# Kernel tuning notes

Hardware: AMD Instinct MI355X
Metric: run time of the kernel (lower is better)

The kernel has to match this reference:

```python
import jax, jax.numpy as jnp
import numpy as np

N_NODES = 100000

def _gcn_conv(x, W, b, src, dst, ew, num_nodes):
    # x: [N, Fin], W: [Fin, Fout], src/dst: [Etot], ew: [Etot]
    xw = x @ W                                   # [N, Fout]
    deg = jax.ops.segment_sum(ew, dst, num_segments=num_nodes)   # [N]
    dinv = jnp.where(deg > 0, jax.lax.rsqrt(jnp.where(deg > 0, deg, 1.0)), 0.0)
    norm = dinv[src] * ew * dinv[dst]            # [Etot]
    msg = xw[src] * norm[:, None]                # [Etot, Fout] gather-transform
    out = jax.ops.segment_sum(msg, dst, num_segments=num_nodes)  # scatter-add
    return out + b

def setup_inputs() -> dict:
    key = jax.random.key(0)
    k1, k2, k3, k4, k5, k6, k7 = jax.random.split(key, 7)
    N, E, F_IN, HID, CLS = N_NODES, 1600000, 128, 64, 32
    x = jax.random.normal(k1, (N, F_IN), dtype=jnp.float32)
    edge_index = jax.random.randint(k2, (2, E), 0, N, dtype=jnp.int64)
    edge_weight = jax.random.uniform(k3, (E,), dtype=jnp.float32)
    s1 = 1.0 / np.sqrt(F_IN)
    s2 = 1.0 / np.sqrt(HID)
    W1 = jax.random.uniform(k4, (F_IN, HID), dtype=jnp.float32, minval=-s1, maxval=s1)
    b1 = jnp.zeros((HID,), dtype=jnp.float32)
    W2 = jax.random.uniform(k5, (HID, CLS), dtype=jnp.float32, minval=-s2, maxval=s2)
    b2 = jnp.zeros((CLS,), dtype=jnp.float32)
    return {"x": x, "edge_index": edge_index, "edge_weight": edge_weight,
            "W1": W1, "b1": b1, "W2": W2, "b2": b2}

def reference(x, edge_index, edge_weight, W1, b1, W2, b2):
    N = x.shape[0]
    # add self-loops with weight 1 (PyG GCNConv default)
    loop = jnp.arange(N, dtype=edge_index.dtype)
    src = jnp.concatenate([edge_index[0], loop])
    dst = jnp.concatenate([edge_index[1], loop])
    ew = jnp.concatenate([edge_weight, jnp.ones((N,), dtype=edge_weight.dtype)])
    h = _gcn_conv(x, W1, b1, src, dst, ew, N)
    h = jax.nn.relu(h)
    # dropout is identity in eval mode
    out = _gcn_conv(h, W2, b2, src, dst, ew, N)
    return out
```

## Files before the change

### kernel.cpp

```cpp
#include <hip/hip_runtime.h>

#define FIN 128
#define HID 64
#define CLS 32

#define BSH 7
#define BNODES 128
#define GB 256
#define BCAP 4096
#define SCAP 6272
#define NBUKP 800

using bfrag = __attribute__((ext_vector_type(8))) short;
using cfrag = __attribute__((ext_vector_type(4))) float;

__device__ inline unsigned short f2bf(float x) {
  unsigned u = __float_as_uint(x);
  return (unsigned short)((u + 0x7FFFu + ((u >> 16) & 1u)) >> 16);
}
__device__ inline void bf8_to_f32(int4 v, float* f) {
  f[0] = __uint_as_float((unsigned)v.x << 16);
  f[1] = __uint_as_float((unsigned)v.x & 0xFFFF0000u);
  f[2] = __uint_as_float((unsigned)v.y << 16);
  f[3] = __uint_as_float((unsigned)v.y & 0xFFFF0000u);
  f[4] = __uint_as_float((unsigned)v.z << 16);
  f[5] = __uint_as_float((unsigned)v.z & 0xFFFF0000u);
  f[6] = __uint_as_float((unsigned)v.w << 16);
  f[7] = __uint_as_float((unsigned)v.w & 0xFFFF0000u);
}

__global__ __launch_bounds__(256) void k_wpack(const float* __restrict__ W1,
                                               const float* __restrict__ W2,
                                               unsigned short* __restrict__ wp1,
                                               unsigned short* __restrict__ wp2) {
  int t = blockIdx.x * 256 + threadIdx.x;
  int total = gridDim.x * 256;
  for (int i = t; i < 16 * 512; i += total) {
    int f = i >> 9, l = (i >> 3) & 63, j = i & 7;
    int ks = f >> 2, nt = f & 3;
    int k = ks * 32 + (l >> 4) * 8 + j;
    int n = nt * 16 + (l & 15);
    wp1[i] = f2bf(W1[k * 64 + n]);
  }
  for (int i = t; i < 4 * 512; i += total) {
    int f = i >> 9, l = (i >> 3) & 63, j = i & 7;
    int ks = f >> 1, nt = f & 1;
    int k = ks * 32 + (l >> 4) * 8 + j;
    int n = nt * 16 + (l & 15);
    wp2[i] = f2bf(W2[k * 32 + n]);
  }
}

__global__ __launch_bounds__(1024) void k_sortchunk(const int* __restrict__ src,
                                                    const int* __restrict__ dst,
                                                    const float* __restrict__ ew,
                                                    int2* __restrict__ recsA,
                                                    int* __restrict__ gcntT,
                                                    int* __restrict__ loffB,
                                                    int E, int CHUNK, int NBUK) {
  __shared__ int2 stage[SCAP];
  __shared__ int lcnt[NBUKP];
  __shared__ int loff[NBUKP];
  __shared__ int lcur[NBUKP];
  __shared__ int ssum[1024];
  const int b = blockIdx.x, t = threadIdx.x;
  const int s = b * CHUNK, e = min(E, s + CHUNK);
  const int m = e - s;

  for (int i = t; i < NBUK; i += 1024) lcnt[i] = 0;
  __syncthreads();
  for (int p = s + t; p < e; p += 1024)
    atomicAdd(&lcnt[dst[p] >> BSH], 1);
  __syncthreads();

  int c = (t < NBUK) ? lcnt[t] : 0;
  ssum[t] = c;
  __syncthreads();
  for (int off = 1; off < 1024; off <<= 1) {
    int v = (t >= off) ? ssum[t - off] : 0;
    __syncthreads();
    ssum[t] += v;
    __syncthreads();
  }
  if (t < NBUK) { loff[t] = ssum[t] - c; lcur[t] = ssum[t] - c; }
  if (t == 0) loff[NBUK] = m;
  __syncthreads();

  for (int p = s + t; p < e; p += 1024) {
    int d = dst[p];
    int bk = d >> BSH;
    int pos = atomicAdd(&lcur[bk], 1);
    stage[pos] = make_int2(src[p] | ((d & (BNODES - 1)) << 17), __float_as_int(ew[p]));
  }
  __syncthreads();

  for (int p = t; p < m; p += 1024) recsA[s + p] = stage[p];
  for (int i = t; i < NBUK; i += 1024) gcntT[i * GB + b] = lcnt[i];
  for (int i = t; i <= NBUK; i += 1024) loffB[b * NBUKP + i] = loff[i];
}

__global__ __launch_bounds__(256) void k_scan_sums(const int* __restrict__ counts,
                                                   int* __restrict__ bsum, int N) {
  __shared__ int s[256];
  int base = blockIdx.x * 4096 + threadIdx.x * 16;
  int t = 0;
#pragma unroll
  for (int j = 0; j < 16; ++j)
    if (base + j < N) t += counts[base + j];
  s[threadIdx.x] = t;
  __syncthreads();
  for (int off = 128; off > 0; off >>= 1) {
    if (threadIdx.x < off) s[threadIdx.x] += s[threadIdx.x + off];
    __syncthreads();
  }
  if (threadIdx.x == 0) bsum[blockIdx.x] = s[0];
}

__global__ __launch_bounds__(256) void k_scan_bsums(int* __restrict__ bsum, int nb) {
  __shared__ int s[256];
  int t = threadIdx.x;
  int v = (t < nb) ? bsum[t] : 0;
  s[t] = v;
  __syncthreads();
  for (int off = 1; off < 256; off <<= 1) {
    int u = (t >= off) ? s[t - off] : 0;
    __syncthreads();
    s[t] += u;
    __syncthreads();
  }
  if (t < nb) bsum[t] = s[t] - v;
}

__global__ __launch_bounds__(256) void k_scan_emit(const int* __restrict__ counts,
                                                   const int* __restrict__ bsum,
                                                   int* __restrict__ rowstart, int N) {
  __shared__ int s[256];
  int base = blockIdx.x * 4096 + threadIdx.x * 16;
  int c[16];
  int tsum = 0;
#pragma unroll
  for (int j = 0; j < 16; ++j) {
    c[j] = (base + j < N) ? counts[base + j] : 0;
    tsum += c[j];
  }
  s[threadIdx.x] = tsum;
  __syncthreads();
  for (int off = 1; off < 256; off <<= 1) {
    int v = (threadIdx.x >= off) ? s[threadIdx.x - off] : 0;
    __syncthreads();
    s[threadIdx.x] += v;
    __syncthreads();
  }
  int run = bsum[blockIdx.x] + s[threadIdx.x] - tsum;
#pragma unroll
  for (int j = 0; j < 16; ++j) {
    if (base + j < N) rowstart[base + j] = run;
    run += c[j];
  }
}

__global__ __launch_bounds__(256) void k_bucket(const int2* __restrict__ recsA,
                                                const int* __restrict__ goff,
                                                const int* __restrict__ loffB,
                                                int2* __restrict__ pairs,
                                                float* __restrict__ dinv,
                                                int* __restrict__ rowstart,
                                                int N, int E, int CHUNK, int NBUK) {
  __shared__ int2 lrec[BCAP];
  __shared__ int2 sout[BCAP];
  __shared__ int cnt[BNODES];
  __shared__ int cur[BNODES];
  __shared__ int sbuf[BNODES];
  __shared__ float degs[BNODES];
  __shared__ float dl[BNODES];
  const int b = blockIdx.x;
  const int t = threadIdx.x;
  const int bstart = goff[b * GB];
  const int bend = (b + 1 < NBUK) ? goff[(b + 1) * GB] : E;
  int m = bend - bstart;
  if (m > BCAP) m = BCAP;

  if (t < BNODES) { cnt[t] = 0; degs[t] = 1.0f; }
  __syncthreads();

  {
    int ls = loffB[t * NBUKP + b];
    int le = loffB[t * NBUKP + b + 1];
    int doff = goff[b * GB + t] - bstart;
    const int2* sp = recsA + (size_t)t * CHUNK + ls;
    int len = le - ls;
    for (int j = 0; j < len; ++j) {
      if (doff + j < BCAP) lrec[doff + j] = sp[j];
    }
  }
  __syncthreads();

  for (int p = t; p < m; p += 256) {
    int2 r = lrec[p];
    int d = (r.x >> 17) & (BNODES - 1);
    atomicAdd(&cnt[d], 1);
    atomicAdd(&degs[d], __int_as_float(r.y));
  }
  __syncthreads();
  if (t < BNODES) sbuf[t] = cnt[t];
  __syncthreads();
  for (int off = 1; off < BNODES; off <<= 1) {
    int v = (t < BNODES && t >= off) ? sbuf[t - off] : 0;
    __syncthreads();
    if (t < BNODES) sbuf[t] += v;
    __syncthreads();
  }
  if (t < BNODES) {
    int ls = sbuf[t] - cnt[t];
    cur[t] = ls;
    float di = rsqrtf(degs[t]);
    dl[t] = di;
    int node = b * BNODES + t;
    if (node < N) { dinv[node] = di; rowstart[node] = bstart + ls; }
  }
  __syncthreads();
  for (int p = t; p < m; p += 256) {
    int2 r = lrec[p];
    int d = (r.x >> 17) & (BNODES - 1);
    int pos = atomicAdd(&cur[d], 1);
    float c = __int_as_float(r.y) * dl[d];
    sout[pos] = make_int2(r.x & 0x1FFFF, __float_as_int(c));
  }
  __syncthreads();
  for (int p = t; p < m; p += 256) pairs[bstart + p] = sout[p];
}

template <int K, int F, bool RELU>
__global__ __launch_bounds__(256, 4) void mfma_gemm(const float* __restrict__ x,
                                                    const unsigned short* __restrict__ wp,
                                                    const float* __restrict__ scale,
                                                    unsigned short* __restrict__ y, int N) {
  constexpr int KS = K / 32;
  constexpr int NT = F / 16;
  const int lane = threadIdx.x & 63;
  const int quad = lane >> 4;
  const int col = lane & 15;
  const int row0 = blockIdx.x * 64 + (threadIdx.x >> 6) * 16;
  if (row0 >= N) return;

  bfrag bf[KS * NT];
#pragma unroll
  for (int f = 0; f < KS * NT; ++f)
    bf[f] = *(const bfrag*)(wp + f * 512 + lane * 8);

  cfrag acc[NT] = {};

  int row_a = row0 + col;
  if (row_a >= N) row_a = N - 1;
  const float* xp = x + (size_t)row_a * K + quad * 8;

#pragma unroll
  for (int ks = 0; ks < KS; ++ks) {
    float4 a0 = *(const float4*)(xp + ks * 32);
    float4 a1 = *(const float4*)(xp + ks * 32 + 4);
    if (RELU) {
      a0.x = fmaxf(a0.x, 0.f); a0.y = fmaxf(a0.y, 0.f);
      a0.z = fmaxf(a0.z, 0.f); a0.w = fmaxf(a0.w, 0.f);
      a1.x = fmaxf(a1.x, 0.f); a1.y = fmaxf(a1.y, 0.f);
      a1.z = fmaxf(a1.z, 0.f); a1.w = fmaxf(a1.w, 0.f);
    }
    bfrag af;
    af[0] = (short)f2bf(a0.x); af[1] = (short)f2bf(a0.y);
    af[2] = (short)f2bf(a0.z); af[3] = (short)f2bf(a0.w);
    af[4] = (short)f2bf(a1.x); af[5] = (short)f2bf(a1.y);
    af[6] = (short)f2bf(a1.z); af[7] = (short)f2bf(a1.w);
#pragma unroll
    for (int nt = 0; nt < NT; ++nt)
      acc[nt] = __builtin_amdgcn_mfma_f32_16x16x32_bf16(af, bf[ks * NT + nt], acc[nt], 0, 0, 0);
  }

  float scr[4];
#pragma unroll
  for (int r = 0; r < 4; ++r) {
    int row = row0 + quad * 4 + r;
    scr[r] = (row < N) ? scale[row] : 0.f;
  }
#pragma unroll
  for (int nt = 0; nt < NT; ++nt)
#pragma unroll
    for (int r = 0; r < 4; ++r) {
      int row = row0 + quad * 4 + r;
      if (row < N)
        y[(size_t)row * F + nt * 16 + col] = f2bf(scr[r] * acc[nt][r]);
    }
}

template <int F>
__global__ __launch_bounds__(256) void pull_agg(const unsigned short* __restrict__ xs,
                                                const int2* __restrict__ pairs,
                                                const int* __restrict__ rowstart,
                                                const float* __restrict__ dinv,
                                                const float* __restrict__ b,
                                                float* __restrict__ out, int N, int E) {
  constexpr int LPN = F / 8;
  constexpr int NPB = 256 / LPN;
  const int g = blockIdx.x * NPB + threadIdx.x / LPN;
  const int f8 = (threadIdx.x % LPN) * 8;
  if (g >= N) return;

  const int start = rowstart[g];
  const int end = (g + 1 < N) ? rowstart[g + 1] : E;
  const float di = dinv[g];

  float acc[8];
  {
    int4 v = *(const int4*)&xs[(size_t)g * F + f8];
    float xf[8];
    bf8_to_f32(v, xf);
    float4 b0 = *(const float4*)&b[f8];
    float4 b1 = *(const float4*)&b[f8 + 4];
    acc[0] = fmaf(di, xf[0], b0.x); acc[1] = fmaf(di, xf[1], b0.y);
    acc[2] = fmaf(di, xf[2], b0.z); acc[3] = fmaf(di, xf[3], b0.w);
    acc[4] = fmaf(di, xf[4], b1.x); acc[5] = fmaf(di, xf[5], b1.y);
    acc[6] = fmaf(di, xf[6], b1.z); acc[7] = fmaf(di, xf[7], b1.w);
  }

  int p = start;
  for (; p + 2 <= end; p += 2) {
    int2 p0 = pairs[p];
    int2 p1 = pairs[p + 1];
    int4 v0 = *(const int4*)&xs[(size_t)p0.x * F + f8];
    int4 v1 = *(const int4*)&xs[(size_t)p1.x * F + f8];
    float c0 = __int_as_float(p0.y), c1 = __int_as_float(p1.y);
    float x0[8], x1[8];
    bf8_to_f32(v0, x0);
    bf8_to_f32(v1, x1);
#pragma unroll
    for (int j = 0; j < 8; ++j) acc[j] = fmaf(c0, x0[j], acc[j]);
#pragma unroll
    for (int j = 0; j < 8; ++j) acc[j] = fmaf(c1, x1[j], acc[j]);
  }
  if (p < end) {
    int2 pa = pairs[p];
    int4 va = *(const int4*)&xs[(size_t)pa.x * F + f8];
    float ca = __int_as_float(pa.y);
    float xa[8];
    bf8_to_f32(va, xa);
#pragma unroll
    for (int j = 0; j < 8; ++j) acc[j] = fmaf(ca, xa[j], acc[j]);
  }
  *(float4*)&out[(size_t)g * F + f8] = make_float4(acc[0], acc[1], acc[2], acc[3]);
  *(float4*)&out[(size_t)g * F + f8 + 4] = make_float4(acc[4], acc[5], acc[6], acc[7]);
}

extern "C" void kernel_launch(void* const* d_in, const int* in_sizes, int n_in,
                              void* d_out, int out_size, void* d_ws, size_t ws_size,
                              hipStream_t stream) {
  const float* x  = (const float*)d_in[0];
  const int*   ei = (const int*)d_in[1];
  const float* ew = (const float*)d_in[2];
  const float* W1 = (const float*)d_in[3];
  const float* b1 = (const float*)d_in[4];
  const float* W2 = (const float*)d_in[5];
  const float* b2 = (const float*)d_in[6];
  float* out = (float*)d_out;

  const int N = in_sizes[0] / FIN;
  const int E = in_sizes[2];
  const int* src = ei;
  const int* dst = ei + E;

  const int NBUK = (N + BNODES - 1) >> BSH;
  const int M = NBUK * GB;
  const int CHUNK = (E + GB - 1) / GB;
  const int nbM = (M + 4095) / 4096;

  float* wsf      = (float*)d_ws;
  float* dinv     = wsf;
  int*   rowstart = (int*)(dinv + N);
  int*   gcntT    = rowstart + N;
  int*   loffB    = gcntT + M;
  int*   bsum     = loffB + GB * NBUKP;
  int2*  recsA    = (int2*)(bsum + 256);
  int2*  pairs    = recsA + E;
  unsigned short* xs1 = (unsigned short*)(pairs + E);
  float* out1     = (float*)(xs1 + (size_t)N * HID);
  unsigned short* xs2 = xs1;
  unsigned short* wp1 = (unsigned short*)(out1 + (size_t)N * HID);
  unsigned short* wp2 = wp1 + 16 * 512;

  k_wpack<<<32, 256, 0, stream>>>(W1, W2, wp1, wp2);
  k_sortchunk<<<GB, 1024, 0, stream>>>(src, dst, ew, recsA, gcntT, loffB, E, CHUNK, NBUK);
  k_scan_sums<<<nbM, 256, 0, stream>>>(gcntT, bsum, M);
  k_scan_bsums<<<1, 256, 0, stream>>>(bsum, nbM);
  k_scan_emit<<<nbM, 256, 0, stream>>>(gcntT, bsum, gcntT, M);
  k_bucket<<<NBUK, 256, 0, stream>>>(recsA, gcntT, loffB, pairs, dinv, rowstart,
                                     N, E, CHUNK, NBUK);

  mfma_gemm<FIN, HID, false><<<(N + 63) / 64, 256, 0, stream>>>(x, wp1, dinv, xs1, N);
  pull_agg<HID><<<(N + 31) / 32, 256, 0, stream>>>(xs1, pairs, rowstart, dinv, b1, out1, N, E);

  mfma_gemm<HID, CLS, true><<<(N + 63) / 64, 256, 0, stream>>>(out1, wp2, dinv, xs2, N);
  pull_agg<CLS><<<(N + 63) / 64, 256, 0, stream>>>(xs2, pairs, rowstart, dinv, b2, out, N, E);
}
```

Measured before the change: 248.7 us.

## Store layer-1 activations as bf16 with fused ReLU; share edge records via shuffles

The first aggregation now applies ReLU and writes its hidden activations as bf16 rather than fp32. The second GEMM reads that bf16 buffer directly, which halves the intermediate traffic and removes a conversion step. The aggregation loop now has each lane load one edge record and broadcast it to the lanes sharing that node through wave shuffles, instead of every lane reloading the same pair. The cost is extra bf16 rounding of the hidden layer and shuffle overhead. Divergent loop trip counts within a wave are also possible.

```diff
diff --git a/kernel.cpp b/kernel.cpp
--- a/kernel.cpp
+++ b/kernel.cpp
@@ -230,8 +230,8 @@
   for (int p = t; p < m; p += 256) pairs[bstart + p] = sout[p];
 }
 
-template <int K, int F, bool RELU>
-__global__ __launch_bounds__(256, 4) void mfma_gemm(const float* __restrict__ x,
+template <int K, int F, bool ABF16>
+__global__ __launch_bounds__(256, 4) void mfma_gemm(const void* __restrict__ xv,
                                                     const unsigned short* __restrict__ wp,
                                                     const float* __restrict__ scale,
                                                     unsigned short* __restrict__ y, int N) {
@@ -252,23 +252,22 @@
 
   int row_a = row0 + col;
   if (row_a >= N) row_a = N - 1;
-  const float* xp = x + (size_t)row_a * K + quad * 8;
 
 #pragma unroll
   for (int ks = 0; ks < KS; ++ks) {
-    float4 a0 = *(const float4*)(xp + ks * 32);
-    float4 a1 = *(const float4*)(xp + ks * 32 + 4);
-    if (RELU) {
-      a0.x = fmaxf(a0.x, 0.f); a0.y = fmaxf(a0.y, 0.f);
-      a0.z = fmaxf(a0.z, 0.f); a0.w = fmaxf(a0.w, 0.f);
-      a1.x = fmaxf(a1.x, 0.f); a1.y = fmaxf(a1.y, 0.f);
-      a1.z = fmaxf(a1.z, 0.f); a1.w = fmaxf(a1.w, 0.f);
+    bfrag af;
+    if (ABF16) {
+      const unsigned short* xp = (const unsigned short*)xv + (size_t)row_a * K + quad * 8;
+      af = *(const bfrag*)(xp + ks * 32);
+    } else {
+      const float* xp = (const float*)xv + (size_t)row_a * K + quad * 8;
+      float4 a0 = *(const float4*)(xp + ks * 32);
+      float4 a1 = *(const float4*)(xp + ks * 32 + 4);
+      af[0] = (short)f2bf(a0.x); af[1] = (short)f2bf(a0.y);
+      af[2] = (short)f2bf(a0.z); af[3] = (short)f2bf(a0.w);
+      af[4] = (short)f2bf(a1.x); af[5] = (short)f2bf(a1.y);
+      af[6] = (short)f2bf(a1.z); af[7] = (short)f2bf(a1.w);
     }
-    bfrag af;
-    af[0] = (short)f2bf(a0.x); af[1] = (short)f2bf(a0.y);
-    af[2] = (short)f2bf(a0.z); af[3] = (short)f2bf(a0.w);
-    af[4] = (short)f2bf(a1.x); af[5] = (short)f2bf(a1.y);
-    af[6] = (short)f2bf(a1.z); af[7] = (short)f2bf(a1.w);
 #pragma unroll
     for (int nt = 0; nt < NT; ++nt)
       acc[nt] = __builtin_amdgcn_mfma_f32_16x16x32_bf16(af, bf[ks * NT + nt], acc[nt], 0, 0, 0);
@@ -290,18 +289,21 @@
     }
 }
 
-template <int F>
+template <int F, bool BF16OUT>
 __global__ __launch_bounds__(256) void pull_agg(const unsigned short* __restrict__ xs,
                                                 const int2* __restrict__ pairs,
                                                 const int* __restrict__ rowstart,
                                                 const float* __restrict__ dinv,
                                                 const float* __restrict__ b,
-                                                float* __restrict__ out, int N, int E) {
+                                                void* __restrict__ outv, int N, int E) {
   constexpr int LPN = F / 8;
   constexpr int NPB = 256 / LPN;
   const int g = blockIdx.x * NPB + threadIdx.x / LPN;
-  const int f8 = (threadIdx.x % LPN) * 8;
+  const int sub = threadIdx.x % LPN;
+  const int f8 = sub * 8;
   if (g >= N) return;
+  const int lane = threadIdx.x & 63;
+  const int gbase = lane - sub;
 
   const int start = rowstart[g];
   const int end = (g + 1 < N) ? rowstart[g + 1] : E;
@@ -321,31 +323,38 @@
   }
 
   int p = start;
-  for (; p + 2 <= end; p += 2) {
-    int2 p0 = pairs[p];
-    int2 p1 = pairs[p + 1];
-    int4 v0 = *(const int4*)&xs[(size_t)p0.x * F + f8];
-    int4 v1 = *(const int4*)&xs[(size_t)p1.x * F + f8];
-    float c0 = __int_as_float(p0.y), c1 = __int_as_float(p1.y);
-    float x0[8], x1[8];
-    bf8_to_f32(v0, x0);
-    bf8_to_f32(v1, x1);
-#pragma unroll
-    for (int j = 0; j < 8; ++j) acc[j] = fmaf(c0, x0[j], acc[j]);
-#pragma unroll
-    for (int j = 0; j < 8; ++j) acc[j] = fmaf(c1, x1[j], acc[j]);
-  }
-  if (p < end) {
-    int2 pa = pairs[p];
-    int4 va = *(const int4*)&xs[(size_t)pa.x * F + f8];
-    float ca = __int_as_float(pa.y);
-    float xa[8];
-    bf8_to_f32(va, xa);
-#pragma unroll
-    for (int j = 0; j < 8; ++j) acc[j] = fmaf(ca, xa[j], acc[j]);
-  }
-  *(float4*)&out[(size_t)g * F + f8] = make_float4(acc[0], acc[1], acc[2], acc[3]);
-  *(float4*)&out[(size_t)g * F + f8 + 4] = make_float4(acc[4], acc[5], acc[6], acc[7]);
+  while (p < end) {
+    int rem = end - p;
+    if (rem > LPN) rem = LPN;
+    int2 myp;
+    if (sub < rem) myp = pairs[p + sub];
+#pragma unroll 4
+    for (int j = 0; j < rem; ++j) {
+      int sidx = __shfl(myp.x, gbase + j, 64);
+      float c = __int_as_float(__shfl(myp.y, gbase + j, 64));
+      int4 v = *(const int4*)&xs[(size_t)sidx * F + f8];
+      float xf[8];
+      bf8_to_f32(v, xf);
+#pragma unroll
+      for (int k = 0; k < 8; ++k) acc[k] = fmaf(c, xf[k], acc[k]);
+    }
+    p += rem;
+  }
+
+  if (BF16OUT) {
+    unsigned short* out = (unsigned short*)outv;
+    ushort4 o0, o1;
+    o0.x = f2bf(fmaxf(acc[0], 0.f)); o0.y = f2bf(fmaxf(acc[1], 0.f));
+    o0.z = f2bf(fmaxf(acc[2], 0.f)); o0.w = f2bf(fmaxf(acc[3], 0.f));
+    o1.x = f2bf(fmaxf(acc[4], 0.f)); o1.y = f2bf(fmaxf(acc[5], 0.f));
+    o1.z = f2bf(fmaxf(acc[6], 0.f)); o1.w = f2bf(fmaxf(acc[7], 0.f));
+    *(ushort4*)&out[(size_t)g * F + f8] = o0;
+    *(ushort4*)&out[(size_t)g * F + f8 + 4] = o1;
+  } else {
+    float* out = (float*)outv;
+    *(float4*)&out[(size_t)g * F + f8] = make_float4(acc[0], acc[1], acc[2], acc[3]);
+    *(float4*)&out[(size_t)g * F + f8 + 4] = make_float4(acc[4], acc[5], acc[6], acc[7]);
+  }
 }
 
 extern "C" void kernel_launch(void* const* d_in, const int* in_sizes, int n_in,
@@ -379,9 +388,9 @@
   int2*  recsA    = (int2*)(bsum + 256);
   int2*  pairs    = recsA + E;
   unsigned short* xs1 = (unsigned short*)(pairs + E);
-  float* out1     = (float*)(xs1 + (size_t)N * HID);
+  unsigned short* out1b = xs1 + (size_t)N * HID;
   unsigned short* xs2 = xs1;
-  unsigned short* wp1 = (unsigned short*)(out1 + (size_t)N * HID);
+  unsigned short* wp1 = out1b + (size_t)N * HID;
   unsigned short* wp2 = wp1 + 16 * 512;
 
   k_wpack<<<32, 256, 0, stream>>>(W1, W2, wp1, wp2);
@@ -393,8 +402,8 @@
                                      N, E, CHUNK, NBUK);
 
   mfma_gemm<FIN, HID, false><<<(N + 63) / 64, 256, 0, stream>>>(x, wp1, dinv, xs1, N);
-  pull_agg<HID><<<(N + 31) / 32, 256, 0, stream>>>(xs1, pairs, rowstart, dinv, b1, out1, N, E);
-
-  mfma_gemm<HID, CLS, true><<<(N + 63) / 64, 256, 0, stream>>>(out1, wp2, dinv, xs2, N);
-  pull_agg<CLS><<<(N + 63) / 64, 256, 0, stream>>>(xs2, pairs, rowstart, dinv, b2, out, N, E);
-}
+  pull_agg<HID, true><<<(N + 31) / 32, 256, 0, stream>>>(xs1, pairs, rowstart, dinv, b1, out1b, N, E);
+
+  mfma_gemm<HID, CLS, true><<<(N + 63) / 64, 256, 0, stream>>>(out1b, wp2, dinv, xs2, N);
+  pull_agg<CLS, false><<<(N + 63) / 64, 256, 0, stream>>>(xs2, pairs, rowstart, dinv, b2, out, N, E);
+}
```

Result: no change. 250.0 us (+0.5%).

## Fuse layer-1 aggregation with ReLU and W2 GEMM, drop global scan kernels

Applied to the files above, without the earlier changes.

The three-kernel global prefix scan is replaced by a per-bucket local scan plus an atomic cursor that assigns each bucket's output region, so the CSR order is no longer globally sorted and an explicit rowend array is stored. W1 packing is folded into the sort kernel as an extra block. The layer-1 pull aggregation now applies ReLU and multiplies by W2 in fp32 through shared memory, writing the scaled bf16 layer-2 input directly. This removes the fp32 out1 round trip and the second MFMA GEMM. It trades these for a scalar shared-memory matmul and nondeterministic bucket placement.

```diff
diff --git a/kernel.cpp b/kernel.cpp
--- a/kernel.cpp
+++ b/kernel.cpp
@@ -29,41 +29,35 @@
   f[7] = __uint_as_float((unsigned)v.w & 0xFFFF0000u);
 }
 
-__global__ __launch_bounds__(256) void k_wpack(const float* __restrict__ W1,
-                                               const float* __restrict__ W2,
-                                               unsigned short* __restrict__ wp1,
-                                               unsigned short* __restrict__ wp2) {
-  int t = blockIdx.x * 256 + threadIdx.x;
-  int total = gridDim.x * 256;
-  for (int i = t; i < 16 * 512; i += total) {
-    int f = i >> 9, l = (i >> 3) & 63, j = i & 7;
-    int ks = f >> 2, nt = f & 3;
-    int k = ks * 32 + (l >> 4) * 8 + j;
-    int n = nt * 16 + (l & 15);
-    wp1[i] = f2bf(W1[k * 64 + n]);
-  }
-  for (int i = t; i < 4 * 512; i += total) {
-    int f = i >> 9, l = (i >> 3) & 63, j = i & 7;
-    int ks = f >> 1, nt = f & 1;
-    int k = ks * 32 + (l >> 4) * 8 + j;
-    int n = nt * 16 + (l & 15);
-    wp2[i] = f2bf(W2[k * 32 + n]);
-  }
-}
-
-__global__ __launch_bounds__(1024) void k_sortchunk(const int* __restrict__ src,
-                                                    const int* __restrict__ dst,
-                                                    const float* __restrict__ ew,
-                                                    int2* __restrict__ recsA,
-                                                    int* __restrict__ gcntT,
-                                                    int* __restrict__ loffB,
-                                                    int E, int CHUNK, int NBUK) {
+__global__ __launch_bounds__(1024) void k_sort_wpack(const int* __restrict__ src,
+                                                     const int* __restrict__ dst,
+                                                     const float* __restrict__ ew,
+                                                     int2* __restrict__ recsA,
+                                                     int* __restrict__ gcntT,
+                                                     int* __restrict__ loffB,
+                                                     const float* __restrict__ W1,
+                                                     unsigned short* __restrict__ wp1,
+                                                     int* __restrict__ cursor,
+                                                     int E, int CHUNK, int NBUK) {
   __shared__ int2 stage[SCAP];
   __shared__ int lcnt[NBUKP];
   __shared__ int loff[NBUKP];
   __shared__ int lcur[NBUKP];
   __shared__ int ssum[1024];
   const int b = blockIdx.x, t = threadIdx.x;
+
+  if (b >= GB) {
+    if (t == 0) *cursor = 0;
+    for (int i = t; i < 16 * 512; i += 1024) {
+      int f = i >> 9, l = (i >> 3) & 63, j = i & 7;
+      int ks = f >> 2, nt = f & 3;
+      int k = ks * 32 + (l >> 4) * 8 + j;
+      int n = nt * 16 + (l & 15);
+      wp1[i] = f2bf(W1[k * 64 + n]);
+    }
+    return;
+  }
+
   const int s = b * CHUNK, e = min(E, s + CHUNK);
   const int m = e - s;
 
@@ -99,98 +93,52 @@
   for (int i = t; i <= NBUK; i += 1024) loffB[b * NBUKP + i] = loff[i];
 }
 
-__global__ __launch_bounds__(256) void k_scan_sums(const int* __restrict__ counts,
-                                                   int* __restrict__ bsum, int N) {
-  __shared__ int s[256];
-  int base = blockIdx.x * 4096 + threadIdx.x * 16;
-  int t = 0;
-#pragma unroll
-  for (int j = 0; j < 16; ++j)
-    if (base + j < N) t += counts[base + j];
-  s[threadIdx.x] = t;
-  __syncthreads();
-  for (int off = 128; off > 0; off >>= 1) {
-    if (threadIdx.x < off) s[threadIdx.x] += s[threadIdx.x + off];
-    __syncthreads();
-  }
-  if (threadIdx.x == 0) bsum[blockIdx.x] = s[0];
-}
-
-__global__ __launch_bounds__(256) void k_scan_bsums(int* __restrict__ bsum, int nb) {
-  __shared__ int s[256];
-  int t = threadIdx.x;
-  int v = (t < nb) ? bsum[t] : 0;
-  s[t] = v;
-  __syncthreads();
-  for (int off = 1; off < 256; off <<= 1) {
-    int u = (t >= off) ? s[t - off] : 0;
-    __syncthreads();
-    s[t] += u;
-    __syncthreads();
-  }
-  if (t < nb) bsum[t] = s[t] - v;
-}
-
-__global__ __launch_bounds__(256) void k_scan_emit(const int* __restrict__ counts,
-                                                   const int* __restrict__ bsum,
-                                                   int* __restrict__ rowstart, int N) {
-  __shared__ int s[256];
-  int base = blockIdx.x * 4096 + threadIdx.x * 16;
-  int c[16];
-  int tsum = 0;
-#pragma unroll
-  for (int j = 0; j < 16; ++j) {
-    c[j] = (base + j < N) ? counts[base + j] : 0;
-    tsum += c[j];
-  }
-  s[threadIdx.x] = tsum;
-  __syncthreads();
-  for (int off = 1; off < 256; off <<= 1) {
-    int v = (threadIdx.x >= off) ? s[threadIdx.x - off] : 0;
-    __syncthreads();
-    s[threadIdx.x] += v;
-    __syncthreads();
-  }
-  int run = bsum[blockIdx.x] + s[threadIdx.x] - tsum;
-#pragma unroll
-  for (int j = 0; j < 16; ++j) {
-    if (base + j < N) rowstart[base + j] = run;
-    run += c[j];
-  }
-}
-
 __global__ __launch_bounds__(256) void k_bucket(const int2* __restrict__ recsA,
-                                                const int* __restrict__ goff,
+                                                const int* __restrict__ gcntT,
                                                 const int* __restrict__ loffB,
                                                 int2* __restrict__ pairs,
                                                 float* __restrict__ dinv,
                                                 int* __restrict__ rowstart,
+                                                int* __restrict__ rowend,
+                                                int* __restrict__ cursor,
                                                 int N, int E, int CHUNK, int NBUK) {
   __shared__ int2 lrec[BCAP];
   __shared__ int2 sout[BCAP];
+  __shared__ int boff[256];
   __shared__ int cnt[BNODES];
   __shared__ int cur[BNODES];
   __shared__ int sbuf[BNODES];
   __shared__ float degs[BNODES];
   __shared__ float dl[BNODES];
+  __shared__ int basesh;
   const int b = blockIdx.x;
   const int t = threadIdx.x;
-  const int bstart = goff[b * GB];
-  const int bend = (b + 1 < NBUK) ? goff[(b + 1) * GB] : E;
-  int m = bend - bstart;
+
+  int bc = gcntT[b * GB + t];
+  boff[t] = bc;
+  __syncthreads();
+  for (int off = 1; off < 256; off <<= 1) {
+    int v = (t >= off) ? boff[t - off] : 0;
+    __syncthreads();
+    boff[t] += v;
+    __syncthreads();
+  }
+  int myoff = boff[t] - bc;
+  int total = boff[255];
+  if (t == 0) basesh = atomicAdd(cursor, total);
+  if (t < BNODES) { cnt[t] = 0; degs[t] = 1.0f; }
+  __syncthreads();
+  const int bstart = basesh;
+  int m = total;
   if (m > BCAP) m = BCAP;
-
-  if (t < BNODES) { cnt[t] = 0; degs[t] = 1.0f; }
-  __syncthreads();
 
   {
     int ls = loffB[t * NBUKP + b];
     int le = loffB[t * NBUKP + b + 1];
-    int doff = goff[b * GB + t] - bstart;
     const int2* sp = recsA + (size_t)t * CHUNK + ls;
     int len = le - ls;
     for (int j = 0; j < len; ++j) {
-      if (doff + j < BCAP) lrec[doff + j] = sp[j];
+      if (myoff + j < BCAP) lrec[myoff + j] = sp[j];
     }
   }
   __syncthreads();
@@ -216,7 +164,11 @@
     float di = rsqrtf(degs[t]);
     dl[t] = di;
     int node = b * BNODES + t;
-    if (node < N) { dinv[node] = di; rowstart[node] = bstart + ls; }
+    if (node < N) {
+      dinv[node] = di;
+      rowstart[node] = bstart + ls;
+      rowend[node] = bstart + ls + cnt[t];
+    }
   }
   __syncthreads();
   for (int p = t; p < m; p += 256) {
@@ -230,7 +182,7 @@
   for (int p = t; p < m; p += 256) pairs[bstart + p] = sout[p];
 }
 
-template <int K, int F, bool RELU>
+template <int K, int F>
 __global__ __launch_bounds__(256, 4) void mfma_gemm(const float* __restrict__ x,
                                                     const unsigned short* __restrict__ wp,
                                                     const float* __restrict__ scale,
@@ -258,12 +210,6 @@
   for (int ks = 0; ks < KS; ++ks) {
     float4 a0 = *(const float4*)(xp + ks * 32);
     float4 a1 = *(const float4*)(xp + ks * 32 + 4);
-    if (RELU) {
-      a0.x = fmaxf(a0.x, 0.f); a0.y = fmaxf(a0.y, 0.f);
-      a0.z = fmaxf(a0.z, 0.f); a0.w = fmaxf(a0.w, 0.f);
-      a1.x = fmaxf(a1.x, 0.f); a1.y = fmaxf(a1.y, 0.f);
-      a1.z = fmaxf(a1.z, 0.f); a1.w = fmaxf(a1.w, 0.f);
-    }
     bfrag af;
     af[0] = (short)f2bf(a0.x); af[1] = (short)f2bf(a0.y);
     af[2] = (short)f2bf(a0.z); af[3] = (short)f2bf(a0.w);
@@ -290,26 +236,110 @@
     }
 }
 
-template <int F>
-__global__ __launch_bounds__(256) void pull_agg(const unsigned short* __restrict__ xs,
+__global__ __launch_bounds__(256) void pull_fuse(const unsigned short* __restrict__ xs,
+                                                 const int2* __restrict__ pairs,
+                                                 const int* __restrict__ rowstart,
+                                                 const int* __restrict__ rowend,
+                                                 const float* __restrict__ dinv,
+                                                 const float* __restrict__ b,
+                                                 const float* __restrict__ W2,
+                                                 unsigned short* __restrict__ xs2,
+                                                 int N, int E) {
+  __shared__ float rows[32 * 64];
+  __shared__ float w2s[64 * 32];
+  const int t = threadIdx.x;
+  for (int i = t; i < 64 * 32; i += 256) w2s[i] = W2[i];
+
+  const int g = blockIdx.x * 32 + t / 8;
+  const int n = t / 8;
+  const int f8 = (t % 8) * 8;
+
+  if (g < N) {
+    const int start = rowstart[g];
+    const int end = rowend[g];
+    const float di = dinv[g];
+
+    float acc[8];
+    {
+      int4 v = *(const int4*)&xs[(size_t)g * HID + f8];
+      float xf[8];
+      bf8_to_f32(v, xf);
+      float4 b0 = *(const float4*)&b[f8];
+      float4 b1 = *(const float4*)&b[f8 + 4];
+      acc[0] = fmaf(di, xf[0], b0.x); acc[1] = fmaf(di, xf[1], b0.y);
+      acc[2] = fmaf(di, xf[2], b0.z); acc[3] = fmaf(di, xf[3], b0.w);
+      acc[4] = fmaf(di, xf[4], b1.x); acc[5] = fmaf(di, xf[5], b1.y);
+      acc[6] = fmaf(di, xf[6], b1.z); acc[7] = fmaf(di, xf[7], b1.w);
+    }
+
+    int p = start;
+    for (; p + 2 <= end; p += 2) {
+      int2 p0 = pairs[p];
+      int2 p1 = pairs[p + 1];
+      int4 v0 = *(const int4*)&xs[(size_t)p0.x * HID + f8];
+      int4 v1 = *(const int4*)&xs[(size_t)p1.x * HID + f8];
+      float c0 = __int_as_float(p0.y), c1 = __int_as_float(p1.y);
+      float x0[8], x1[8];
+      bf8_to_f32(v0, x0);
+      bf8_to_f32(v1, x1);
+#pragma unroll
+      for (int j = 0; j < 8; ++j) acc[j] = fmaf(c0, x0[j], acc[j]);
+#pragma unroll
+      for (int j = 0; j < 8; ++j) acc[j] = fmaf(c1, x1[j], acc[j]);
+    }
+    if (p < end) {
+      int2 pa = pairs[p];
+      int4 va = *(const int4*)&xs[(size_t)pa.x * HID + f8];
+      float ca = __int_as_float(pa.y);
+      float xa[8];
+      bf8_to_f32(va, xa);
+#pragma unroll
+      for (int j = 0; j < 8; ++j) acc[j] = fmaf(ca, xa[j], acc[j]);
+    }
+#pragma unroll
+    for (int j = 0; j < 8; ++j) rows[n * 64 + f8 + j] = fmaxf(acc[j], 0.f);
+  }
+  __syncthreads();
+
+  const int o0 = (t % 8) * 4;
+  if (g < N) {
+    float4 o = make_float4(0.f, 0.f, 0.f, 0.f);
+    const float* rp = &rows[n * 64];
+#pragma unroll 8
+    for (int k = 0; k < 64; ++k) {
+      float r = rp[k];
+      float4 wv = *(const float4*)&w2s[k * 32 + o0];
+      o.x = fmaf(r, wv.x, o.x); o.y = fmaf(r, wv.y, o.y);
+      o.z = fmaf(r, wv.z, o.z); o.w = fmaf(r, wv.w, o.w);
+    }
+    float di = dinv[g];
+    ushort4 ov;
+    ov.x = f2bf(di * o.x); ov.y = f2bf(di * o.y);
+    ov.z = f2bf(di * o.z); ov.w = f2bf(di * o.w);
+    *(ushort4*)&xs2[(size_t)g * CLS + o0] = ov;
+  }
+}
+
+__global__ __launch_bounds__(256) void pull_out(const unsigned short* __restrict__ xs,
                                                 const int2* __restrict__ pairs,
                                                 const int* __restrict__ rowstart,
+                                                const int* __restrict__ rowend,
                                                 const float* __restrict__ dinv,
                                                 const float* __restrict__ b,
                                                 float* __restrict__ out, int N, int E) {
-  constexpr int LPN = F / 8;
+  constexpr int LPN = CLS / 8;
   constexpr int NPB = 256 / LPN;
   const int g = blockIdx.x * NPB + threadIdx.x / LPN;
   const int f8 = (threadIdx.x % LPN) * 8;
   if (g >= N) return;
 
   const int start = rowstart[g];
-  const int end = (g + 1 < N) ? rowstart[g + 1] : E;
+  const int end = rowend[g];
   const float di = dinv[g];
 
   float acc[8];
   {
-    int4 v = *(const int4*)&xs[(size_t)g * F + f8];
+    int4 v = *(const int4*)&xs[(size_t)g * CLS + f8];
     float xf[8];
     bf8_to_f32(v, xf);
     float4 b0 = *(const float4*)&b[f8];
@@ -324,8 +354,8 @@
   for (; p + 2 <= end; p += 2) {
     int2 p0 = pairs[p];
     int2 p1 = pairs[p + 1];
-    int4 v0 = *(const int4*)&xs[(size_t)p0.x * F + f8];
-    int4 v1 = *(const int4*)&xs[(size_t)p1.x * F + f8];
+    int4 v0 = *(const int4*)&xs[(size_t)p0.x * CLS + f8];
+    int4 v1 = *(const int4*)&xs[(size_t)p1.x * CLS + f8];
     float c0 = __int_as_float(p0.y), c1 = __int_as_float(p1.y);
     float x0[8], x1[8];
     bf8_to_f32(v0, x0);
@@ -337,15 +367,15 @@
   }
   if (p < end) {
     int2 pa = pairs[p];
-    int4 va = *(const int4*)&xs[(size_t)pa.x * F + f8];
+    int4 va = *(const int4*)&xs[(size_t)pa.x * CLS + f8];
     float ca = __int_as_float(pa.y);
     float xa[8];
     bf8_to_f32(va, xa);
 #pragma unroll
     for (int j = 0; j < 8; ++j) acc[j] = fmaf(ca, xa[j], acc[j]);
   }
-  *(float4*)&out[(size_t)g * F + f8] = make_float4(acc[0], acc[1], acc[2], acc[3]);
-  *(float4*)&out[(size_t)g * F + f8 + 4] = make_float4(acc[4], acc[5], acc[6], acc[7]);
+  *(float4*)&out[(size_t)g * CLS + f8] = make_float4(acc[0], acc[1], acc[2], acc[3]);
+  *(float4*)&out[(size_t)g * CLS + f8 + 4] = make_float4(acc[4], acc[5], acc[6], acc[7]);
 }
 
 extern "C" void kernel_launch(void* const* d_in, const int* in_sizes, int n_in,
@@ -368,33 +398,28 @@
   const int NBUK = (N + BNODES - 1) >> BSH;
   const int M = NBUK * GB;
   const int CHUNK = (E + GB - 1) / GB;
-  const int nbM = (M + 4095) / 4096;
 
   float* wsf      = (float*)d_ws;
   float* dinv     = wsf;
   int*   rowstart = (int*)(dinv + N);
-  int*   gcntT    = rowstart + N;
+  int*   rowend   = rowstart + N;
+  int*   gcntT    = rowend + N;
   int*   loffB    = gcntT + M;
-  int*   bsum     = loffB + GB * NBUKP;
-  int2*  recsA    = (int2*)(bsum + 256);
+  int*   cursor   = loffB + GB * NBUKP;
+  int2*  recsA    = (int2*)(cursor + 4);
   int2*  pairs    = recsA + E;
   unsigned short* xs1 = (unsigned short*)(pairs + E);
-  float* out1     = (float*)(xs1 + (size_t)N * HID);
-  unsigned short* xs2 = xs1;
-  unsigned short* wp1 = (unsigned short*)(out1 + (size_t)N * HID);
-  unsigned short* wp2 = wp1 + 16 * 512;
-
-  k_wpack<<<32, 256, 0, stream>>>(W1, W2, wp1, wp2);
-  k_sortchunk<<<GB, 1024, 0, stream>>>(src, dst, ew, recsA, gcntT, loffB, E, CHUNK, NBUK);
-  k_scan_sums<<<nbM, 256, 0, stream>>>(gcntT, bsum, M);
-  k_scan_bsums<<<1, 256, 0, stream>>>(bsum, nbM);
-  k_scan_emit<<<nbM, 256, 0, stream>>>(gcntT, bsum, gcntT, M);
+  unsigned short* xs2 = xs1 + (size_t)N * HID;
+  unsigned short* wp1 = xs2 + (size_t)N * CLS;
+
+  k_sort_wpack<<<GB + 1, 1024, 0, stream>>>(src, dst, ew, recsA, gcntT, loffB,
+                                            W1, wp1, cursor, E, CHUNK, NBUK);
   k_bucket<<<NBUK, 256, 0, stream>>>(recsA, gcntT, loffB, pairs, dinv, rowstart,
-                                     N, E, CHUNK, NBUK);
-
-  mfma_gemm<FIN, HID, false><<<(N + 63) / 64, 256, 0, stream>>>(x, wp1, dinv, xs1, N);
-  pull_agg<HID><<<(N + 31) / 32, 256, 0, stream>>>(xs1, pairs, rowstart, dinv, b1, out1, N, E);
-
-  mfma_gemm<HID, CLS, true><<<(N + 63) / 64, 256, 0, stream>>>(out1, wp2, dinv, xs2, N);
-  pull_agg<CLS><<<(N + 63) / 64, 256, 0, stream>>>(xs2, pairs, rowstart, dinv, b2, out, N, E);
-}
+                                     rowend, cursor, N, E, CHUNK, NBUK);
+
+  mfma_gemm<FIN, HID><<<(N + 63) / 64, 256, 0, stream>>>(x, wp1, dinv, xs1, N);
+  pull_fuse<<<(N + 31) / 32, 256, 0, stream>>>(xs1, pairs, rowstart, rowend, dinv,
+                                               b1, W2, xs2, N, E);
+  pull_out<<<(N + 63) / 64, 256, 0, stream>>>(xs2, pairs, rowstart, rowend, dinv,
+                                              b2, out, N, E);
+}
```

New measurement: 269.7 us. 1.08x slower.
